# Kernel tuning notes

Hardware: AMD Instinct MI355X
Metric: run time of the kernel (lower is better)

Reference implementation:

```python
import jax, jax.numpy as jnp
import numpy as np

N = 50000   # nodes per graph
F = 128     # num_features (== hidden width 128 in GCNConv stack)
G = 3       # number_graphs
E = 600000  # edges per graph


def setup_inputs() -> dict:
    key = jax.random.key(0)
    ks = jax.random.split(key, 16)
    s = 0.05  # glorot-ish scale for 128-wide layers
    inp = {
        "x": jax.random.normal(ks[0], (G, N, F), jnp.float32),
        "fc1_w": jax.random.normal(ks[1], (G, F, F), jnp.float32) * s,
        "fc1_b": jnp.zeros((G, F), jnp.float32),
        "w_conv1": jax.random.normal(ks[2], (F, 128), jnp.float32) * s,
        "b_conv1": jnp.zeros((128,), jnp.float32),
        "w_conv2": jax.random.normal(ks[3], (128, 128), jnp.float32) * s,
        "b_conv2": jnp.zeros((128,), jnp.float32),
        "w_dconv1": jax.random.normal(ks[4], (128, 128), jnp.float32) * s,
        "b_dconv1": jnp.zeros((128,), jnp.float32),
        "w_dconv2": jax.random.normal(ks[5], (128, F), jnp.float32) * s,
        "b_dconv2": jnp.zeros((F,), jnp.float32),
        "fc2_w": jax.random.normal(ks[6], (2 * F, F), jnp.float32) * s,
        "fc2_b": jnp.zeros((F,), jnp.float32),
        "att_w": jax.random.normal(ks[7], (G, 128, 128), jnp.float32) * s,
        "edge_index": jax.random.randint(ks[8], (G, 2, E), 0, N, jnp.int64),
    }
    return inp


def _gcn(x, src, dst, W, b):
    # PyG GCNConv: add self-loops, symmetric D^-1/2 (A+I) D^-1/2 normalization
    n = x.shape[0]
    h = x @ W                                  # [N, out]
    loops = jnp.arange(n)
    s = jnp.concatenate([src, loops])
    d = jnp.concatenate([dst, loops])
    deg = jax.ops.segment_sum(jnp.ones_like(d, dtype=h.dtype), d, num_segments=n)
    dinv = jnp.where(deg > 0, jax.lax.rsqrt(deg), 0.0)
    norm = dinv[s] * dinv[d]                   # [E+N]
    out = jax.ops.segment_sum(h[s] * norm[:, None], d, num_segments=n)
    return out + b


_gcn_g = jax.vmap(_gcn, in_axes=(0, 0, 0, None, None))  # over graphs (shared weights)


def _fro(a):
    # Frobenius norm over last two axes (matches torch.norm(., p=2) on a matrix)
    return jnp.sqrt(jnp.sum(a * a, axis=(-2, -1)))


def reference(x, fc1_w, fc1_b, w_conv1, b_conv1, w_conv2, b_conv2,
              w_dconv1, b_dconv1, w_dconv2, b_dconv2, fc2_w, fc2_b,
              att_w, edge_index):
    g = x.shape[0]
    src, dst = edge_index[:, 0], edge_index[:, 1]

    # per-graph fc1 (distinct weights per graph)
    pre_feat = jnp.einsum('gnf,gfo->gno', x, fc1_w) + fc1_b[:, None, :]
    conv1_f = _gcn_g(pre_feat, src, dst, w_conv1, b_conv1)   # [G,N,128]
    enc = _gcn_g(conv1_f, src, dst, w_conv2, b_conv2)        # encoder_H [G,N,128]

    global_vec = jax.nn.sigmoid(jnp.mean(enc, axis=1))       # [G,128]

    # leave-one-out decoder input: (sum_j enc_j - enc_i) / (G-1)
    dec_in = (jnp.sum(enc, axis=0)[None] - enc) / (g - 1)

    own1 = _gcn_g(enc, src, dst, w_dconv1, b_dconv1)         # decov1_f
    own2 = _gcn_g(own1, src, dst, w_dconv2, b_dconv2)        # reconstructed x
    oth1 = _gcn_g(dec_in, src, dst, w_dconv1, b_dconv1)
    oth2 = _gcn_g(oth1, src, dst, w_dconv2, b_dconv2)

    fuse_h = jnp.concatenate([own2, oth2], axis=-1)          # [G,N,2F]
    each_fin = jnp.einsum('gnf,fo->gno', fuse_h, fc2_w) + fc2_b  # [G,N,F]

    # cross-graph attention: sigmoid(H_j @ W_i @ g_i) for all (i, j)
    u = jnp.einsum('ide,ie->id', att_w, global_vec)          # W_i @ g_i -> [G,128]
    S = jax.nn.sigmoid(jnp.einsum('jnd,id->ijn', enc, u))    # [i,j,n]
    L = jnp.transpose(S, (0, 2, 1))                          # [i,n,j]
    L = L / jnp.sum(L, axis=-1, keepdims=True)               # row-normalize over j
    comp_re = jnp.transpose(L, (1, 0, 2)).reshape(x.shape[1], g * g)  # [N, G*G]

    fuse_feat = jax.nn.sigmoid(jnp.mean(each_fin, axis=0))   # [N,F]
    used_feat = jax.nn.elu(jnp.mean(enc, axis=0))            # [N,128]

    obf1 = jnp.sum((_fro(pre_feat - own2) + _fro(conv1_f - own1)) / 2)
    obf0 = jnp.float32(0.0)
    for i in range(g):
        for j in range(g):
            if i != j:
                obf0 = obf0 + _fro(each_fin[i] - each_fin[j])
    return (fuse_feat, used_feat, comp_re, obf1, obf0)
```

## Files before the change

kernel.cpp:

```cpp
#include <hip/hip_runtime.h>

#define NN 50000
#define NFEAT 128
#define NG 3
#define NE 600000

typedef unsigned int u32;
typedef unsigned short u16;
typedef __bf16 bf16x8 __attribute__((ext_vector_type(8)));
typedef float f32x4 __attribute__((ext_vector_type(4)));

__device__ __forceinline__ u16 f2bf(float f){
  u32 u = __float_as_uint(f);
  return (u16)((u + 0x7fffu + ((u >> 16) & 1u)) >> 16);
}
__device__ __forceinline__ float bf2f(u32 s){
  return __uint_as_float((s & 0xffffu) << 16);
}
__device__ __forceinline__ u32 pack2(float a, float b){
  return (u32)f2bf(a) | ((u32)f2bf(b) << 16);
}
__device__ __forceinline__ float sigm(float x){ return 1.f / (1.f + __expf(-x)); }

__global__ void wprep_kernel(const float* fc1w, const float* wc1, const float* wc2,
                             const float* wd1, const float* wd2, const float* fc2w,
                             u16* WT){
  int idx = blockIdx.x * 256 + threadIdx.x;
  if (idx >= 147456) return;
  float v;
  if (idx < 49152){
    int g = idx / 16384, r = idx % 16384; int o = r / 128, f = r % 128;
    v = fc1w[g * 16384 + f * 128 + o];
  } else if (idx < 114688){
    int m = (idx - 49152) / 16384, r = (idx - 49152) % 16384;
    int o = r / 128, f = r % 128;
    const float* w = (m == 0) ? wc1 : (m == 1) ? wc2 : (m == 2) ? wd1 : wd2;
    v = w[f * 128 + o];
  } else {
    int r = idx - 114688; int half = r / 16384; r %= 16384;
    int o = r / 128, f = r % 128;
    v = fc2w[(half * 128 + f) * 128 + o];
  }
  WT[idx] = f2bf(v);
}

__global__ void deg_kernel(const int* ei, int* deg){
  int t = blockIdx.x * 256 + threadIdx.x;
  if (t >= NG * NE) return;
  int g = t / NE, e = t - g * NE;
  int dst = ei[(size_t)g * 2 * NE + NE + e];
  atomicAdd(deg + (size_t)g * NN + dst, 1);
}

__global__ __launch_bounds__(1024) void scan_kernel(const int* deg, int* rowptr, float* dinv){
  const int g = blockIdx.x;
  const int* d = deg + (size_t)g * NN;
  int* rp = rowptr + g * (NN + 1);
  float* di = dinv + (size_t)g * NN;
  __shared__ int s[1024];
  __shared__ int carry;
  if (threadIdx.x == 0) carry = 0;
  __syncthreads();
  for (int base = 0; base <= NN; base += 1024){
    int idx = base + threadIdx.x;
    int v = (idx < NN) ? d[idx] : 0;
    if (idx < NN) di[idx] = rsqrtf((float)(v + 1));
    s[threadIdx.x] = v;
    __syncthreads();
    for (int off = 1; off < 1024; off <<= 1){
      int x = (threadIdx.x >= off) ? s[threadIdx.x - off] : 0;
      __syncthreads();
      s[threadIdx.x] += x;
      __syncthreads();
    }
    int incl = s[threadIdx.x];
    int run = carry;
    if (idx <= NN) rp[idx] = run + incl - v;
    __syncthreads();
    if (threadIdx.x == 1023) carry = run + s[1023];
    __syncthreads();
  }
}

__global__ void fill_kernel(const int* ei, const int* rowptr, int* cursor, int* colbuf){
  int t = blockIdx.x * 256 + threadIdx.x;
  if (t >= NG * NE) return;
  int g = t / NE, e = t - g * NE;
  int src = ei[(size_t)g * 2 * NE + e];
  int dst = ei[(size_t)g * 2 * NE + NE + e];
  int pos = atomicAdd(cursor + (size_t)g * NN + dst, 1);
  colbuf[(size_t)g * NE + rowptr[g * (NN + 1) + dst] + pos] = src;
}

template<int MODE>
__global__ __launch_bounds__(256, 2) void gemm_kernel(
    const void* Ap, const void* Ap2, const u16* W, const u16* W2,
    const float* bias, u16* Out, const float* scale,
    int wPerG, int biasPerG, int hasBias, int outStride16, int outOff16, int aPerG)
{
  __shared__ __align__(16) unsigned char sA[128 * 256];
  __shared__ __align__(16) unsigned char sW[128 * 256];
  const int tid = threadIdx.x;
  const int g = blockIdx.y;
  const int nb = blockIdx.x * 128;
  const int lane = tid & 63, wv = tid >> 6;
  const int wm = (wv & 1) * 64, wn = (wv >> 1) * 64;
  const int l15 = lane & 15, lh = lane >> 4;
  f32x4 acc[4][4] = {};
  constexpr int passes = (MODE == 3) ? 2 : 1;
  for (int p = 0; p < passes; p++){
    if (p) __syncthreads();
    {
      const u16* wsrc = (p ? W2 : W) + (wPerG ? g * 16384 : 0);
      const uint4* w4 = (const uint4*)wsrc;
      for (int i = tid; i < 2048; i += 256){
        int r = i >> 4, c = i & 15;
        uint4 v = w4[i];
        *(uint4*)(sW + r * 256 + ((c * 16) ^ ((r & 7) << 4))) = v;
      }
    }
    if (MODE == 1){
      const float* xp = (const float*)Ap + (size_t)g * NN * NFEAT;
      for (int i = tid; i < 2048; i += 256){
        int r = i >> 4, c = i & 15; int node = nb + r;
        uint4 o = {0, 0, 0, 0};
        if (node < NN){
          const float* row = xp + (size_t)node * NFEAT + c * 8;
          float4 a4 = *(const float4*)row;
          float4 b4 = *(const float4*)(row + 4);
          o.x = pack2(a4.x, a4.y); o.y = pack2(a4.z, a4.w);
          o.z = pack2(b4.x, b4.y); o.w = pack2(b4.z, b4.w);
        }
        *(uint4*)(sA + r * 256 + ((c * 16) ^ ((r & 7) << 4))) = o;
      }
    } else {
      const u16* asrc = (const u16*)(p ? Ap2 : Ap) + (aPerG ? (size_t)g * NN * NFEAT : 0);
      const uint4* a4 = (const uint4*)asrc;
      for (int i = tid; i < 2048; i += 256){
        int r = i >> 4, c = i & 15; int node = nb + r;
        uint4 v = {0, 0, 0, 0};
        if (node < NN) v = a4[(size_t)node * 16 + c];
        *(uint4*)(sA + r * 256 + ((c * 16) ^ ((r & 7) << 4))) = v;
      }
    }
    __syncthreads();
    #pragma unroll
    for (int k0 = 0; k0 < 128; k0 += 32){
      const int kb = 2 * (k0 + lh * 8);
      bf16x8 af[4], bfr[4];
      #pragma unroll
      for (int t = 0; t < 4; t++){
        int rm = wm + t * 16 + l15;
        af[t] = *reinterpret_cast<const bf16x8*>(sW + rm * 256 + (kb ^ ((rm & 7) << 4)));
        int rn = wn + t * 16 + l15;
        bfr[t] = *reinterpret_cast<const bf16x8*>(sA + rn * 256 + (kb ^ ((rn & 7) << 4)));
      }
      #pragma unroll
      for (int mi = 0; mi < 4; mi++)
        #pragma unroll
        for (int ni = 0; ni < 4; ni++)
          acc[mi][ni] = __builtin_amdgcn_mfma_f32_16x16x32_bf16(af[mi], bfr[ni], acc[mi][ni], 0, 0, 0);
    }
  }
  float scn[4] = {1.f, 1.f, 1.f, 1.f};
  if (scale){
    const float* sg = scale + (size_t)g * NN;
    #pragma unroll
    for (int ni = 0; ni < 4; ni++){
      int node = nb + wn + ni * 16 + l15;
      scn[ni] = (node < NN) ? sg[node] : 0.f;
    }
  }
  u16* outg = Out + (size_t)g * NN * outStride16;
  #pragma unroll
  for (int mi = 0; mi < 4; mi++){
    int mbase = wm + mi * 16 + lh * 4;
    f32x4 bv = {};
    if (hasBias) bv = *reinterpret_cast<const f32x4*>(bias + (biasPerG ? g * NFEAT : 0) + mbase);
    #pragma unroll
    for (int ni = 0; ni < 4; ni++){
      int node = nb + wn + ni * 16 + l15;
      if (node < NN){
        f32x4 v = acc[mi][ni];
        float s = scn[ni];
        ushort4 o;
        o.x = f2bf((v.x + bv.x) * s); o.y = f2bf((v.y + bv.y) * s);
        o.z = f2bf((v.z + bv.z) * s); o.w = f2bf((v.w + bv.w) * s);
        *reinterpret_cast<ushort4*>(outg + (size_t)node * outStride16 + outOff16 + mbase) = o;
      }
    }
  }
}

__global__ __launch_bounds__(256) void agg_kernel(
    const u16* H, u16* Outp, const float* bias, const float* dinv,
    const int* rowptr, const int* colidx)
{
  const int g = blockIdx.y;
  const int v = blockIdx.x * 4 + (threadIdx.x >> 6);
  const int l = threadIdx.x & 63;
  const int q = l >> 4, sub = l & 15;
  const uint4* h4 = (const uint4*)(H + (size_t)g * NN * NFEAT);
  const int* rp = rowptr + g * (NN + 1);
  const int* ci = colidx + (size_t)g * NE;
  const int e0 = rp[v];
  const int nslot = rp[v + 1] - e0 + 1;
  float aa[8] = {0,0,0,0,0,0,0,0};
  const int nIter = (nslot + 7) >> 3;
  for (int it = 0; it < nIter; ++it){
    int sA = it * 8 + q;
    int sB = sA + 4;
    int srcA = (sA == 0) ? v : ((sA < nslot) ? ci[e0 + sA - 1] : v);
    int srcB = (sB < nslot) ? ci[e0 + sB - 1] : v;
    uint4 hA = h4[(size_t)srcA * 16 + sub];
    uint4 hB = h4[(size_t)srcB * 16 + sub];
    if (sA < nslot){
      aa[0] += bf2f(hA.x); aa[1] += bf2f(hA.x >> 16);
      aa[2] += bf2f(hA.y); aa[3] += bf2f(hA.y >> 16);
      aa[4] += bf2f(hA.z); aa[5] += bf2f(hA.z >> 16);
      aa[6] += bf2f(hA.w); aa[7] += bf2f(hA.w >> 16);
    }
    if (sB < nslot){
      aa[0] += bf2f(hB.x); aa[1] += bf2f(hB.x >> 16);
      aa[2] += bf2f(hB.y); aa[3] += bf2f(hB.y >> 16);
      aa[4] += bf2f(hB.z); aa[5] += bf2f(hB.z >> 16);
      aa[6] += bf2f(hB.w); aa[7] += bf2f(hB.w >> 16);
    }
  }
  #pragma unroll
  for (int i = 0; i < 8; i++){
    aa[i] += __shfl_xor(aa[i], 16);
    aa[i] += __shfl_xor(aa[i], 32);
  }
  if (q == 0){
    const float dvv = dinv[(size_t)g * NN + v];
    const float4 b4a = *(const float4*)(bias + sub * 8);
    const float4 b4b = *(const float4*)(bias + sub * 8 + 4);
    uint4 o;
    o.x = pack2(aa[0] * dvv + b4a.x, aa[1] * dvv + b4a.y);
    o.y = pack2(aa[2] * dvv + b4a.z, aa[3] * dvv + b4a.w);
    o.z = pack2(aa[4] * dvv + b4b.x, aa[5] * dvv + b4b.y);
    o.w = pack2(aa[6] * dvv + b4b.z, aa[7] * dvv + b4b.w);
    ((uint4*)(Outp + (size_t)g * NN * NFEAT))[(size_t)v * 16 + sub] = o;
  }
}

template<int COMB, bool SQ>
__global__ __launch_bounds__(256) void agg2_kernel(
    const u16* F, u16* OutOwn, u16* OutOth, const float* bias, const float* dinv,
    const int* rowptr, const int* colidx, const u16* Ref, float* sqslot)
{
  const int g = blockIdx.y;
  const int v = blockIdx.x * 4 + (threadIdx.x >> 6);
  const int l = threadIdx.x & 63;
  const int q = l >> 4, sub = l & 15;
  const uint4* h4 = (const uint4*)(F + (size_t)g * NN * 256);
  const int* rp = rowptr + g * (NN + 1);
  const int* ci = colidx + (size_t)g * NE;
  const int e0 = rp[v];
  const int nslot = rp[v + 1] - e0 + 1;
  float uu[8] = {0,0,0,0,0,0,0,0};
  float tt[8] = {0,0,0,0,0,0,0,0};
  const int nIter = (nslot + 7) >> 3;
  for (int it = 0; it < nIter; ++it){
    int sA = it * 8 + q;
    int sB = sA + 4;
    int srcA = (sA == 0) ? v : ((sA < nslot) ? ci[e0 + sA - 1] : v);
    int srcB = (sB < nslot) ? ci[e0 + sB - 1] : v;
    uint4 uA = h4[(size_t)srcA * 32 + sub];
    uint4 tA = h4[(size_t)srcA * 32 + 16 + sub];
    uint4 uB = h4[(size_t)srcB * 32 + sub];
    uint4 tB = h4[(size_t)srcB * 32 + 16 + sub];
    if (sA < nslot){
      uu[0] += bf2f(uA.x); uu[1] += bf2f(uA.x >> 16);
      uu[2] += bf2f(uA.y); uu[3] += bf2f(uA.y >> 16);
      uu[4] += bf2f(uA.z); uu[5] += bf2f(uA.z >> 16);
      uu[6] += bf2f(uA.w); uu[7] += bf2f(uA.w >> 16);
      tt[0] += bf2f(tA.x); tt[1] += bf2f(tA.x >> 16);
      tt[2] += bf2f(tA.y); tt[3] += bf2f(tA.y >> 16);
      tt[4] += bf2f(tA.z); tt[5] += bf2f(tA.z >> 16);
      tt[6] += bf2f(tA.w); tt[7] += bf2f(tA.w >> 16);
    }
    if (sB < nslot){
      uu[0] += bf2f(uB.x); uu[1] += bf2f(uB.x >> 16);
      uu[2] += bf2f(uB.y); uu[3] += bf2f(uB.y >> 16);
      uu[4] += bf2f(uB.z); uu[5] += bf2f(uB.z >> 16);
      uu[6] += bf2f(uB.w); uu[7] += bf2f(uB.w >> 16);
      tt[0] += bf2f(tB.x); tt[1] += bf2f(tB.x >> 16);
      tt[2] += bf2f(tB.y); tt[3] += bf2f(tB.y >> 16);
      tt[4] += bf2f(tB.z); tt[5] += bf2f(tB.z >> 16);
      tt[6] += bf2f(tB.w); tt[7] += bf2f(tB.w >> 16);
    }
  }
  #pragma unroll
  for (int i = 0; i < 8; i++){
    uu[i] += __shfl_xor(uu[i], 16); uu[i] += __shfl_xor(uu[i], 32);
    tt[i] += __shfl_xor(tt[i], 16); tt[i] += __shfl_xor(tt[i], 32);
  }
  const float dvv = dinv[(size_t)g * NN + v];
  const float4 b4a = *(const float4*)(bias + sub * 8);
  const float4 b4b = *(const float4*)(bias + sub * 8 + 4);
  float own[8], oth[8];
  const float bb[8] = {b4a.x, b4a.y, b4a.z, b4a.w, b4b.x, b4b.y, b4b.z, b4b.w};
  #pragma unroll
  for (int i = 0; i < 8; i++){
    own[i] = uu[i] * dvv + bb[i];
    if (COMB) oth[i] = (tt[i] - uu[i]) * dvv * 0.5f + bb[i];
    else      oth[i] = tt[i] * dvv + bb[i];
  }
  float sq = 0.f;
  if (q == 0){
    if (SQ){
      uint4 rv = ((const uint4*)(Ref + (size_t)g * NN * NFEAT))[(size_t)v * 16 + sub];
      float d;
      d = bf2f(rv.x) - own[0]; sq += d * d; d = bf2f(rv.x >> 16) - own[1]; sq += d * d;
      d = bf2f(rv.y) - own[2]; sq += d * d; d = bf2f(rv.y >> 16) - own[3]; sq += d * d;
      d = bf2f(rv.z) - own[4]; sq += d * d; d = bf2f(rv.z >> 16) - own[5]; sq += d * d;
      d = bf2f(rv.w) - own[6]; sq += d * d; d = bf2f(rv.w >> 16) - own[7]; sq += d * d;
    }
    uint4 o;
    o.x = pack2(own[0], own[1]); o.y = pack2(own[2], own[3]);
    o.z = pack2(own[4], own[5]); o.w = pack2(own[6], own[7]);
    ((uint4*)(OutOwn + (size_t)g * NN * NFEAT))[(size_t)v * 16 + sub] = o;
    uint4 o2;
    o2.x = pack2(oth[0], oth[1]); o2.y = pack2(oth[2], oth[3]);
    o2.z = pack2(oth[4], oth[5]); o2.w = pack2(oth[6], oth[7]);
    ((uint4*)(OutOth + (size_t)g * NN * NFEAT))[(size_t)v * 16 + sub] = o2;
  }
  if (SQ){
    __shared__ float red[4];
    sq += __shfl_xor(sq, 1); sq += __shfl_xor(sq, 2);
    sq += __shfl_xor(sq, 4); sq += __shfl_xor(sq, 8);
    if (l == 0) red[threadIdx.x >> 6] = sq;
    __syncthreads();
    if (threadIdx.x == 0)
      atomicAdd(sqslot + g, red[0] + red[1] + red[2] + red[3]);
  }
}

__global__ __launch_bounds__(256) void encsum_kernel(
    const u16* Enc, u16* EncSum, float* outUsed, float* colsum)
{
  const int fp = threadIdx.x & 63, sub = threadIdx.x >> 6;
  const u32* e0 = (const u32*)Enc;
  const u32* e1 = e0 + (size_t)NN * 64;
  const u32* e2 = e1 + (size_t)NN * 64;
  u32* es = (u32*)EncSum;
  float cs[6] = {0, 0, 0, 0, 0, 0};
  for (int v = blockIdx.x * 4 + sub; v < NN; v += gridDim.x * 4){
    size_t idx = (size_t)v * 64 + fp;
    u32 a = e0[idx], b = e1[idx], c = e2[idx];
    float axv = bf2f(a), ayv = bf2f(a >> 16);
    float bxv = bf2f(b), byv = bf2f(b >> 16);
    float cxv = bf2f(c), cyv = bf2f(c >> 16);
    cs[0] += axv; cs[1] += ayv; cs[2] += bxv; cs[3] += byv; cs[4] += cxv; cs[5] += cyv;
    float sx = axv + bxv + cxv, sy = ayv + byv + cyv;
    es[idx] = pack2(sx, sy);
    float ux = sx * (1.f / 3.f), uy = sy * (1.f / 3.f);
    float2 o;
    o.x = ux > 0.f ? ux : expm1f(ux);
    o.y = uy > 0.f ? uy : expm1f(uy);
    *(float2*)(outUsed + (size_t)v * NFEAT + 2 * fp) = o;
  }
  __shared__ float red[256];
  #pragma unroll
  for (int q = 0; q < 6; q++){
    red[threadIdx.x] = cs[q];
    __syncthreads();
    if (sub == 0){
      float s = red[fp] + red[64 + fp] + red[128 + fp] + red[192 + fp];
      atomicAdd(&colsum[(q >> 1) * NFEAT + 2 * fp + (q & 1)], s);
    }
    __syncthreads();
  }
}

__global__ void gvecu_kernel(const float* colsum, const float* att, float* u){
  __shared__ float gv[3 * 128];
  const int t = threadIdx.x;
  for (int g = 0; g < 3; g++) gv[g * 128 + t] = sigm(colsum[g * 128 + t] * (1.f / 50000.f));
  __syncthreads();
  for (int i = 0; i < 3; i++){
    float s = 0.f;
    for (int e = 0; e < 128; e++)
      s += att[(size_t)i * 16384 + (size_t)t * 128 + e] * gv[i * 128 + e];
    u[i * 128 + t] = s;
  }
}

__global__ __launch_bounds__(256) void fuse_kernel(const u16* EF, float* outFuse, float* slots){
  const int fp = threadIdx.x & 63, sub = threadIdx.x >> 6;
  const u32* e0 = (const u32*)EF;
  const u32* e1 = e0 + (size_t)NN * 64;
  const u32* e2 = e1 + (size_t)NN * 64;
  float s01 = 0, s02 = 0, s12 = 0;
  for (int v = blockIdx.x * 4 + sub; v < NN; v += gridDim.x * 4){
    size_t idx = (size_t)v * 64 + fp;
    u32 a = e0[idx], b = e1[idx], c = e2[idx];
    float axv = bf2f(a), ayv = bf2f(a >> 16), bxv = bf2f(b), byv = bf2f(b >> 16);
    float cxv = bf2f(c), cyv = bf2f(c >> 16);
    float2 o;
    o.x = sigm((axv + bxv + cxv) * (1.f / 3.f));
    o.y = sigm((ayv + byv + cyv) * (1.f / 3.f));
    *(float2*)(outFuse + (size_t)v * NFEAT + 2 * fp) = o;
    float dx, dy;
    dx = axv - bxv; dy = ayv - byv; s01 += dx * dx + dy * dy;
    dx = axv - cxv; dy = ayv - cyv; s02 += dx * dx + dy * dy;
    dx = bxv - cxv; dy = byv - cyv; s12 += dx * dx + dy * dy;
  }
  __shared__ float red[256];
  float vals[3] = {s01, s02, s12};
  #pragma unroll
  for (int q = 0; q < 3; q++){
    red[threadIdx.x] = vals[q];
    __syncthreads();
    for (int s2 = 128; s2 > 0; s2 >>= 1){
      if (threadIdx.x < s2) red[threadIdx.x] += red[threadIdx.x + s2];
      __syncthreads();
    }
    if (threadIdx.x == 0) atomicAdd(slots + 6 + q, red[0]);
    __syncthreads();
  }
}

__global__ __launch_bounds__(256) void comp_kernel(const u16* Enc, const float* u, float* outC){
  __shared__ float su[384];
  for (int i = threadIdx.x; i < 384; i += 256) su[i] = u[i];
  __syncthreads();
  const int v = blockIdx.x * 4 + (threadIdx.x >> 6);
  const int l = threadIdx.x & 63;
  const u32* e = (const u32*)Enc;
  float ex[3], ey[3];
  #pragma unroll
  for (int j = 0; j < 3; j++){
    u32 t = e[((size_t)j * NN + v) * 64 + l];
    ex[j] = bf2f(t); ey[j] = bf2f(t >> 16);
  }
  float p[9];
  #pragma unroll
  for (int i = 0; i < 3; i++){
    float uxi = su[i * 128 + 2 * l], uyi = su[i * 128 + 2 * l + 1];
    #pragma unroll
    for (int j = 0; j < 3; j++)
      p[i * 3 + j] = ex[j] * uxi + ey[j] * uyi;
  }
  #pragma unroll
  for (int q = 0; q < 9; q++){
    float s = p[q];
    #pragma unroll
    for (int off = 1; off < 64; off <<= 1) s += __shfl_xor(s, off, 64);
    p[q] = s;
  }
  if (l < 9){
    float sg[9];
    #pragma unroll
    for (int q = 0; q < 9; q++) sg[q] = sigm(p[q]);
    float d0 = sg[0] + sg[1] + sg[2], d1 = sg[3] + sg[4] + sg[5], d2 = sg[6] + sg[7] + sg[8];
    float num = sg[0];
    if (l == 1) num = sg[1]; if (l == 2) num = sg[2]; if (l == 3) num = sg[3];
    if (l == 4) num = sg[4]; if (l == 5) num = sg[5]; if (l == 6) num = sg[6];
    if (l == 7) num = sg[7]; if (l == 8) num = sg[8];
    float den = (l < 3) ? d0 : (l < 6) ? d1 : d2;
    outC[(size_t)v * 9 + l] = num / den;
  }
}

__global__ void final_kernel(const float* slots, float* out){
  if (threadIdx.x == 0){
    float obf1 = 0.f;
    for (int g = 0; g < 3; g++)
      obf1 += 0.5f * (sqrtf(slots[3 + g]) + sqrtf(slots[g]));
    float obf0 = 2.f * (sqrtf(slots[6]) + sqrtf(slots[7]) + sqrtf(slots[8]));
    out[13250000] = obf1;
    out[13250001] = obf0;
  }
}

extern "C" void kernel_launch(void* const* d_in, const int* in_sizes, int n_in,
                              void* d_out, int out_size, void* d_ws, size_t ws_size,
                              hipStream_t stream)
{
  (void)in_sizes; (void)n_in; (void)out_size;
  const float* x    = (const float*)d_in[0];
  const float* fc1w = (const float*)d_in[1];
  const float* fc1b = (const float*)d_in[2];
  const float* wc1  = (const float*)d_in[3];
  const float* bc1  = (const float*)d_in[4];
  const float* wc2  = (const float*)d_in[5];
  const float* bc2  = (const float*)d_in[6];
  const float* wd1  = (const float*)d_in[7];
  const float* bd1  = (const float*)d_in[8];
  const float* wd2  = (const float*)d_in[9];
  const float* bd2  = (const float*)d_in[10];
  const float* fc2w = (const float*)d_in[11];
  const float* fc2b = (const float*)d_in[12];
  const float* attw = (const float*)d_in[13];
  const int*   ei   = (const int*)d_in[14];
  float* out = (float*)d_out;
  char* ws = (char*)d_ws;

  constexpr size_t BUFB = (size_t)NG * NN * NFEAT * 2;
  u16* WT   = (u16*)(ws + 0);
  u16* buf0 = (u16*)(ws + 327680);
  u16* buf1 = (u16*)(ws + 327680 + 1 * BUFB);
  u16* buf2 = (u16*)(ws + 327680 + 2 * BUFB);
  u16* bufT = (u16*)(ws + 327680 + 3 * BUFB);
  u16* bufF = (u16*)(ws + 327680 + 4 * BUFB);
  size_t off = 327680 + 6 * BUFB;
  u16* encsum = (u16*)(ws + off); off += (size_t)NN * NFEAT * 2;
  float* dinv = (float*)(ws + off); off += (size_t)NG * NN * 4;
  int* rowptr = (int*)(ws + off); off += 600064;
  int* colbuf = (int*)(ws + off); off += (size_t)NG * NE * 4;
  size_t zero_off = off;
  int* deg     = (int*)(ws + off); off += (size_t)NG * NN * 4;
  int* cursor  = (int*)(ws + off); off += (size_t)NG * NN * 4;
  float* colsum = (float*)(ws + off); off += 1536;
  float* slots  = (float*)(ws + off); off += 64;
  size_t zero_bytes = off - zero_off;
  float* uvec = (float*)(ws + off); off += 1536;
  if (ws_size < off) return;

  hipMemsetAsync(ws + zero_off, 0, zero_bytes, stream);

  wprep_kernel<<<576, 256, 0, stream>>>(fc1w, wc1, wc2, wd1, wd2, fc2w, WT);
  deg_kernel<<<7032, 256, 0, stream>>>(ei, deg);
  scan_kernel<<<NG, 1024, 0, stream>>>(deg, rowptr, dinv);
  fill_kernel<<<7032, 256, 0, stream>>>(ei, rowptr, cursor, colbuf);

  const u16* WT_fc1 = WT;
  const u16* WT_c1  = WT + 49152;
  const u16* WT_c2  = WT + 65536;
  const u16* WT_d1  = WT + 81920;
  const u16* WT_d2  = WT + 98304;
  const u16* WT_f2a = WT + 114688;
  const u16* WT_f2b = WT + 131072;
  dim3 gg(391, NG), ag(12500, NG);

  gemm_kernel<1><<<gg, 256, 0, stream>>>(x, nullptr, WT_fc1, nullptr, fc1b, buf0, nullptr, 1, 1, 1, 128, 0, 1);
  gemm_kernel<0><<<gg, 256, 0, stream>>>(buf0, nullptr, WT_c1, nullptr, nullptr, bufT, dinv, 0, 0, 0, 128, 0, 1);
  agg_kernel<<<ag, 256, 0, stream>>>(bufT, buf1, bc1, dinv, rowptr, colbuf);
  gemm_kernel<0><<<gg, 256, 0, stream>>>(buf1, nullptr, WT_c2, nullptr, nullptr, bufT, dinv, 0, 0, 0, 128, 0, 1);
  agg_kernel<<<ag, 256, 0, stream>>>(bufT, buf2, bc2, dinv, rowptr, colbuf);
  encsum_kernel<<<256, 256, 0, stream>>>(buf2, encsum, out + 6400000, colsum);
  gvecu_kernel<<<1, 128, 0, stream>>>(colsum, attw, uvec);
  gemm_kernel<0><<<gg, 256, 0, stream>>>(buf2, nullptr, WT_d1, nullptr, nullptr, bufF, dinv, 0, 0, 0, 256, 0, 1);
  gemm_kernel<0><<<gg, 256, 0, stream>>>(encsum, nullptr, WT_d1, nullptr, nullptr, bufF, dinv, 0, 0, 0, 256, 128, 0);
  agg2_kernel<1, true><<<ag, 256, 0, stream>>>(bufF, bufT, buf1, bd1, dinv, rowptr, colbuf, buf1, slots + 0);
  gemm_kernel<0><<<gg, 256, 0, stream>>>(bufT, nullptr, WT_d2, nullptr, nullptr, bufF, dinv, 0, 0, 0, 256, 0, 1);
  gemm_kernel<0><<<gg, 256, 0, stream>>>(buf1, nullptr, WT_d2, nullptr, nullptr, bufF, dinv, 0, 0, 0, 256, 128, 1);
  agg2_kernel<0, true><<<ag, 256, 0, stream>>>(bufF, buf0, buf1, bd2, dinv, rowptr, colbuf, buf0, slots + 3);
  gemm_kernel<3><<<gg, 256, 0, stream>>>(buf0, buf1, WT_f2a, WT_f2b, fc2b, bufF, nullptr, 0, 0, 1, 128, 0, 1);
  fuse_kernel<<<256, 256, 0, stream>>>(bufF, out, slots);
  comp_kernel<<<12500, 256, 0, stream>>>(buf2, uvec, out + 12800000);
  final_kernel<<<1, 64, 0, stream>>>(slots, out);
}
```

Measured before the change: 1.946 ms.

## Sort CSR neighbor lists and walk aggregation by source-node tiles

A new sort_kernel insertion-sorts each node's neighbor list by source index. It also records per-node byte offsets that split those neighbors into 16 source-range tiles. The aggregation kernels now walk neighbors tile by tile, and the self-loop is added separately instead of through the interleaved two-slot loop. The aim is better gather locality in L2 when reading neighbor feature rows. The cost is an extra preprocessing pass, 16 short inner loops per node with little memory-level parallelism, and a u8 offset format that assumes node degree stays under 256.

```diff
diff --git a/kernel.cpp b/kernel.cpp
--- a/kernel.cpp
+++ b/kernel.cpp
@@ -4,9 +4,12 @@
 #define NFEAT 128
 #define NG 3
 #define NE 600000
+#define NTILE 16
+#define TILEW 3125
 
 typedef unsigned int u32;
 typedef unsigned short u16;
+typedef unsigned char u8;
 typedef __bf16 bf16x8 __attribute__((ext_vector_type(8)));
 typedef float f32x4 __attribute__((ext_vector_type(4)));
 
@@ -90,6 +93,28 @@
   int dst = ei[(size_t)g * 2 * NE + NE + e];
   int pos = atomicAdd(cursor + (size_t)g * NN + dst, 1);
   colbuf[(size_t)g * NE + rowptr[g * (NN + 1) + dst] + pos] = src;
+}
+
+__global__ void sort_kernel(const int* rowptr, int* colbuf, u8* toff){
+  int idx = blockIdx.x * 256 + threadIdx.x;
+  if (idx >= NG * NN) return;
+  int g = idx / NN, v = idx - g * NN;
+  const int* rp = rowptr + g * (NN + 1);
+  int base = rp[v], deg = rp[v + 1] - rp[v];
+  int* a = colbuf + (size_t)g * NE + base;
+  for (int i = 1; i < deg; i++){
+    int key = a[i]; int j = i - 1;
+    while (j >= 0 && a[j] > key){ a[j + 1] = a[j]; j--; }
+    a[j + 1] = key;
+  }
+  u8* tb = toff + (size_t)idx * (NTILE + 1);
+  tb[0] = 0;
+  int ti = 1;
+  for (int i = 0; i < deg; i++){
+    int s = a[i];
+    while (ti < NTILE + 1 && s >= ti * TILEW){ tb[ti] = (u8)i; ti++; }
+  }
+  while (ti < NTILE + 1){ tb[ti] = (u8)deg; ti++; }
 }
 
 template<int MODE>
@@ -194,7 +219,7 @@
 
 __global__ __launch_bounds__(256) void agg_kernel(
     const u16* H, u16* Outp, const float* bias, const float* dinv,
-    const int* rowptr, const int* colidx)
+    const int* rowptr, const int* colidx, const u8* toff)
 {
   const int g = blockIdx.y;
   const int v = blockIdx.x * 4 + (threadIdx.x >> 6);
@@ -204,28 +229,26 @@
   const int* rp = rowptr + g * (NN + 1);
   const int* ci = colidx + (size_t)g * NE;
   const int e0 = rp[v];
-  const int nslot = rp[v + 1] - e0 + 1;
-  float aa[8] = {0,0,0,0,0,0,0,0};
-  const int nIter = (nslot + 7) >> 3;
-  for (int it = 0; it < nIter; ++it){
-    int sA = it * 8 + q;
-    int sB = sA + 4;
-    int srcA = (sA == 0) ? v : ((sA < nslot) ? ci[e0 + sA - 1] : v);
-    int srcB = (sB < nslot) ? ci[e0 + sB - 1] : v;
-    uint4 hA = h4[(size_t)srcA * 16 + sub];
-    uint4 hB = h4[(size_t)srcB * 16 + sub];
-    if (sA < nslot){
-      aa[0] += bf2f(hA.x); aa[1] += bf2f(hA.x >> 16);
-      aa[2] += bf2f(hA.y); aa[3] += bf2f(hA.y >> 16);
-      aa[4] += bf2f(hA.z); aa[5] += bf2f(hA.z >> 16);
-      aa[6] += bf2f(hA.w); aa[7] += bf2f(hA.w >> 16);
-    }
-    if (sB < nslot){
-      aa[0] += bf2f(hB.x); aa[1] += bf2f(hB.x >> 16);
-      aa[2] += bf2f(hB.y); aa[3] += bf2f(hB.y >> 16);
-      aa[4] += bf2f(hB.z); aa[5] += bf2f(hB.z >> 16);
-      aa[6] += bf2f(hB.w); aa[7] += bf2f(hB.w >> 16);
-    }
+  const u8* tv = toff + ((size_t)g * NN + v) * (NTILE + 1);
+  float aa[8] = {0, 0, 0, 0, 0, 0, 0, 0};
+  #pragma unroll 1
+  for (int t = 0; t < NTILE; t++){
+    const int lo = e0 + tv[t], hi = e0 + tv[t + 1];
+    for (int s = lo + q; s < hi; s += 4){
+      int src = ci[s];
+      uint4 hh = h4[(size_t)src * 16 + sub];
+      aa[0] += bf2f(hh.x); aa[1] += bf2f(hh.x >> 16);
+      aa[2] += bf2f(hh.y); aa[3] += bf2f(hh.y >> 16);
+      aa[4] += bf2f(hh.z); aa[5] += bf2f(hh.z >> 16);
+      aa[6] += bf2f(hh.w); aa[7] += bf2f(hh.w >> 16);
+    }
+  }
+  if (q == 0){
+    uint4 hv = h4[(size_t)v * 16 + sub];
+    aa[0] += bf2f(hv.x); aa[1] += bf2f(hv.x >> 16);
+    aa[2] += bf2f(hv.y); aa[3] += bf2f(hv.y >> 16);
+    aa[4] += bf2f(hv.z); aa[5] += bf2f(hv.z >> 16);
+    aa[6] += bf2f(hv.w); aa[7] += bf2f(hv.w >> 16);
   }
   #pragma unroll
   for (int i = 0; i < 8; i++){
@@ -248,7 +271,7 @@
 template<int COMB, bool SQ>
 __global__ __launch_bounds__(256) void agg2_kernel(
     const u16* F, u16* OutOwn, u16* OutOth, const float* bias, const float* dinv,
-    const int* rowptr, const int* colidx, const u16* Ref, float* sqslot)
+    const int* rowptr, const int* colidx, const u8* toff, const u16* Ref, float* sqslot)
 {
   const int g = blockIdx.y;
   const int v = blockIdx.x * 4 + (threadIdx.x >> 6);
@@ -258,39 +281,37 @@
   const int* rp = rowptr + g * (NN + 1);
   const int* ci = colidx + (size_t)g * NE;
   const int e0 = rp[v];
-  const int nslot = rp[v + 1] - e0 + 1;
-  float uu[8] = {0,0,0,0,0,0,0,0};
-  float tt[8] = {0,0,0,0,0,0,0,0};
-  const int nIter = (nslot + 7) >> 3;
-  for (int it = 0; it < nIter; ++it){
-    int sA = it * 8 + q;
-    int sB = sA + 4;
-    int srcA = (sA == 0) ? v : ((sA < nslot) ? ci[e0 + sA - 1] : v);
-    int srcB = (sB < nslot) ? ci[e0 + sB - 1] : v;
-    uint4 uA = h4[(size_t)srcA * 32 + sub];
-    uint4 tA = h4[(size_t)srcA * 32 + 16 + sub];
-    uint4 uB = h4[(size_t)srcB * 32 + sub];
-    uint4 tB = h4[(size_t)srcB * 32 + 16 + sub];
-    if (sA < nslot){
-      uu[0] += bf2f(uA.x); uu[1] += bf2f(uA.x >> 16);
-      uu[2] += bf2f(uA.y); uu[3] += bf2f(uA.y >> 16);
-      uu[4] += bf2f(uA.z); uu[5] += bf2f(uA.z >> 16);
-      uu[6] += bf2f(uA.w); uu[7] += bf2f(uA.w >> 16);
-      tt[0] += bf2f(tA.x); tt[1] += bf2f(tA.x >> 16);
-      tt[2] += bf2f(tA.y); tt[3] += bf2f(tA.y >> 16);
-      tt[4] += bf2f(tA.z); tt[5] += bf2f(tA.z >> 16);
-      tt[6] += bf2f(tA.w); tt[7] += bf2f(tA.w >> 16);
-    }
-    if (sB < nslot){
-      uu[0] += bf2f(uB.x); uu[1] += bf2f(uB.x >> 16);
-      uu[2] += bf2f(uB.y); uu[3] += bf2f(uB.y >> 16);
-      uu[4] += bf2f(uB.z); uu[5] += bf2f(uB.z >> 16);
-      uu[6] += bf2f(uB.w); uu[7] += bf2f(uB.w >> 16);
-      tt[0] += bf2f(tB.x); tt[1] += bf2f(tB.x >> 16);
-      tt[2] += bf2f(tB.y); tt[3] += bf2f(tB.y >> 16);
-      tt[4] += bf2f(tB.z); tt[5] += bf2f(tB.z >> 16);
-      tt[6] += bf2f(tB.w); tt[7] += bf2f(tB.w >> 16);
-    }
+  const u8* tv = toff + ((size_t)g * NN + v) * (NTILE + 1);
+  float uu[8] = {0, 0, 0, 0, 0, 0, 0, 0};
+  float tt[8] = {0, 0, 0, 0, 0, 0, 0, 0};
+  #pragma unroll 1
+  for (int t = 0; t < NTILE; t++){
+    const int lo = e0 + tv[t], hi = e0 + tv[t + 1];
+    for (int s = lo + q; s < hi; s += 4){
+      int src = ci[s];
+      uint4 ua = h4[(size_t)src * 32 + sub];
+      uint4 ta = h4[(size_t)src * 32 + 16 + sub];
+      uu[0] += bf2f(ua.x); uu[1] += bf2f(ua.x >> 16);
+      uu[2] += bf2f(ua.y); uu[3] += bf2f(ua.y >> 16);
+      uu[4] += bf2f(ua.z); uu[5] += bf2f(ua.z >> 16);
+      uu[6] += bf2f(ua.w); uu[7] += bf2f(ua.w >> 16);
+      tt[0] += bf2f(ta.x); tt[1] += bf2f(ta.x >> 16);
+      tt[2] += bf2f(ta.y); tt[3] += bf2f(ta.y >> 16);
+      tt[4] += bf2f(ta.z); tt[5] += bf2f(ta.z >> 16);
+      tt[6] += bf2f(ta.w); tt[7] += bf2f(ta.w >> 16);
+    }
+  }
+  if (q == 0){
+    uint4 uv = h4[(size_t)v * 32 + sub];
+    uint4 tvv = h4[(size_t)v * 32 + 16 + sub];
+    uu[0] += bf2f(uv.x); uu[1] += bf2f(uv.x >> 16);
+    uu[2] += bf2f(uv.y); uu[3] += bf2f(uv.y >> 16);
+    uu[4] += bf2f(uv.z); uu[5] += bf2f(uv.z >> 16);
+    uu[6] += bf2f(uv.w); uu[7] += bf2f(uv.w >> 16);
+    tt[0] += bf2f(tvv.x); tt[1] += bf2f(tvv.x >> 16);
+    tt[2] += bf2f(tvv.y); tt[3] += bf2f(tvv.y >> 16);
+    tt[4] += bf2f(tvv.z); tt[5] += bf2f(tvv.z >> 16);
+    tt[6] += bf2f(tvv.w); tt[7] += bf2f(tvv.w >> 16);
   }
   #pragma unroll
   for (int i = 0; i < 8; i++){
@@ -300,8 +321,8 @@
   const float dvv = dinv[(size_t)g * NN + v];
   const float4 b4a = *(const float4*)(bias + sub * 8);
   const float4 b4b = *(const float4*)(bias + sub * 8 + 4);
+  const float bb[8] = {b4a.x, b4a.y, b4a.z, b4a.w, b4b.x, b4b.y, b4b.z, b4b.w};
   float own[8], oth[8];
-  const float bb[8] = {b4a.x, b4a.y, b4a.z, b4a.w, b4b.x, b4b.y, b4b.z, b4b.w};
   #pragma unroll
   for (int i = 0; i < 8; i++){
     own[i] = uu[i] * dvv + bb[i];
@@ -511,6 +532,7 @@
   float* dinv = (float*)(ws + off); off += (size_t)NG * NN * 4;
   int* rowptr = (int*)(ws + off); off += 600064;
   int* colbuf = (int*)(ws + off); off += (size_t)NG * NE * 4;
+  u8* toff = (u8*)(ws + off); off += (size_t)NG * NN * (NTILE + 1);
   size_t zero_off = off;
   int* deg     = (int*)(ws + off); off += (size_t)NG * NN * 4;
   int* cursor  = (int*)(ws + off); off += (size_t)NG * NN * 4;
@@ -526,6 +548,7 @@
   deg_kernel<<<7032, 256, 0, stream>>>(ei, deg);
   scan_kernel<<<NG, 1024, 0, stream>>>(deg, rowptr, dinv);
   fill_kernel<<<7032, 256, 0, stream>>>(ei, rowptr, cursor, colbuf);
+  sort_kernel<<<586, 256, 0, stream>>>(rowptr, colbuf, toff);
 
   const u16* WT_fc1 = WT;
   const u16* WT_c1  = WT + 49152;
@@ -538,17 +561,17 @@
 
   gemm_kernel<1><<<gg, 256, 0, stream>>>(x, nullptr, WT_fc1, nullptr, fc1b, buf0, nullptr, 1, 1, 1, 128, 0, 1);
   gemm_kernel<0><<<gg, 256, 0, stream>>>(buf0, nullptr, WT_c1, nullptr, nullptr, bufT, dinv, 0, 0, 0, 128, 0, 1);
-  agg_kernel<<<ag, 256, 0, stream>>>(bufT, buf1, bc1, dinv, rowptr, colbuf);
+  agg_kernel<<<ag, 256, 0, stream>>>(bufT, buf1, bc1, dinv, rowptr, colbuf, toff);
   gemm_kernel<0><<<gg, 256, 0, stream>>>(buf1, nullptr, WT_c2, nullptr, nullptr, bufT, dinv, 0, 0, 0, 128, 0, 1);
-  agg_kernel<<<ag, 256, 0, stream>>>(bufT, buf2, bc2, dinv, rowptr, colbuf);
+  agg_kernel<<<ag, 256, 0, stream>>>(bufT, buf2, bc2, dinv, rowptr, colbuf, toff);
   encsum_kernel<<<256, 256, 0, stream>>>(buf2, encsum, out + 6400000, colsum);
   gvecu_kernel<<<1, 128, 0, stream>>>(colsum, attw, uvec);
   gemm_kernel<0><<<gg, 256, 0, stream>>>(buf2, nullptr, WT_d1, nullptr, nullptr, bufF, dinv, 0, 0, 0, 256, 0, 1);
   gemm_kernel<0><<<gg, 256, 0, stream>>>(encsum, nullptr, WT_d1, nullptr, nullptr, bufF, dinv, 0, 0, 0, 256, 128, 0);
-  agg2_kernel<1, true><<<ag, 256, 0, stream>>>(bufF, bufT, buf1, bd1, dinv, rowptr, colbuf, buf1, slots + 0);
+  agg2_kernel<1, true><<<ag, 256, 0, stream>>>(bufF, bufT, buf1, bd1, dinv, rowptr, colbuf, toff, buf1, slots + 0);
   gemm_kernel<0><<<gg, 256, 0, stream>>>(bufT, nullptr, WT_d2, nullptr, nullptr, bufF, dinv, 0, 0, 0, 256, 0, 1);
   gemm_kernel<0><<<gg, 256, 0, stream>>>(buf1, nullptr, WT_d2, nullptr, nullptr, bufF, dinv, 0, 0, 0, 256, 128, 1);
-  agg2_kernel<0, true><<<ag, 256, 0, stream>>>(bufF, buf0, buf1, bd2, dinv, rowptr, colbuf, buf0, slots + 3);
+  agg2_kernel<0, true><<<ag, 256, 0, stream>>>(bufF, buf0, buf1, bd2, dinv, rowptr, colbuf, toff, buf0, slots + 3);
   gemm_kernel<3><<<gg, 256, 0, stream>>>(buf0, buf1, WT_f2a, WT_f2b, fc2b, bufF, nullptr, 0, 0, 1, 128, 0, 1);
   fuse_kernel<<<256, 256, 0, stream>>>(bufF, out, slots);
   comp_kernel<<<12500, 256, 0, stream>>>(buf2, uvec, out + 12800000);
```

Result: slower. 2.378 ms (+22.2%).
